# Kernel optimization log

Measured on AMD Instinct MI355X. Metric: run time of the kernel, lower is better.

## Reference

```python
import jax, jax.numpy as jnp
import numpy as np

DIM = 768
HEADS = 12
DH = DIM // HEADS
HIDDEN = 4 * DIM
EPS = 1e-5


def layernorm(x, g, b):
    mu = jnp.mean(x, axis=-1, keepdims=True)
    var = jnp.mean(jnp.square(x - mu), axis=-1, keepdims=True)
    return (x - mu) * jax.lax.rsqrt(var + EPS) * g + b


def setup_inputs() -> dict:
    key = jax.random.key(0)
    ks = jax.random.split(key, 12)
    B, N = 8, 1024
    s_in = 1.0 / np.sqrt(DIM)
    s_hid = 1.0 / np.sqrt(HIDDEN)
    return {
        "x": jax.random.normal(ks[0], (B, N, DIM), jnp.float32),
        "q_extra": jax.random.normal(ks[1], (B, N, DIM), jnp.float32),
        "ln1_g": jnp.ones((DIM,), jnp.float32),
        "ln1_b": jnp.zeros((DIM,), jnp.float32),
        "w_kv": jax.random.normal(ks[2], (DIM, 2 * DIM), jnp.float32) * s_in,
        "w_out": jax.random.normal(ks[3], (DIM, DIM), jnp.float32) * s_in,
        "b_out": jnp.zeros((DIM,), jnp.float32),
        "ln2_g": jnp.ones((DIM,), jnp.float32),
        "ln2_b": jnp.zeros((DIM,), jnp.float32),
        "w1": jax.random.normal(ks[4], (DIM, HIDDEN), jnp.float32) * s_in,
        "b1": jnp.zeros((HIDDEN,), jnp.float32),
        "w2": jax.random.normal(ks[5], (HIDDEN, DIM), jnp.float32) * s_hid,
        "b2": jnp.zeros((DIM,), jnp.float32),
    }


def reference(x, q_extra, ln1_g, ln1_b, w_kv, w_out, b_out, ln2_g, ln2_b, w1, b1, w2, b2):
    B, N, C = x.shape
    scale = DH ** (-0.5)

    # pre-norm cross attention
    xn = layernorm(x, ln1_g, ln1_b)
    kv = (xn @ w_kv).reshape(B, N, 2, HEADS, DH)
    k = kv[:, :, 0]  # [B,N,H,Dh]
    v = kv[:, :, 1]
    q = q_extra.reshape(B, N, HEADS, DH)
    dots = jnp.einsum('bnhd,bmhd->bhnm', q, k) * scale
    attn = jax.nn.softmax(dots, axis=-1)
    out = jnp.einsum('bhnm,bmhd->bnhd', attn, v).reshape(B, N, C)
    out = out @ w_out + b_out

    x = x + out  # residual

    # pre-norm MLP
    h = layernorm(x, ln2_g, ln2_b)
    h = jax.nn.gelu(h @ w1 + b1, approximate=False)
    h = h @ w2 + b2
    return x + h
```

## Files before the change

kernel.cpp:

```cpp
#include <hip/hip_runtime.h>
#include <math.h>

typedef __attribute__((ext_vector_type(8))) short short8;
typedef __attribute__((ext_vector_type(8))) _Float16 half8;
typedef __attribute__((ext_vector_type(2))) __fp16 fp16x2;
typedef __attribute__((ext_vector_type(4))) float float4v;
typedef __attribute__((ext_vector_type(4))) unsigned short ushort4v;

__device__ __forceinline__ unsigned short f2bf(float f) {
  union { unsigned int i; float f; } x; x.f = f;
  unsigned int r = x.i + 0x7fffu + ((x.i >> 16) & 1u);
  return (unsigned short)(r >> 16);
}

__device__ __forceinline__ float gelu_f(float y) {
  const float z = fabsf(y) * 0.70710678118654752f;
  const float t = 1.0f / (1.0f + 0.3275911f * z);
  const float poly = t * (0.254829592f + t * (-0.284496736f +
                     t * (1.421413741f + t * (-1.453152027f + t * 1.061405429f))));
  const float e = exp2f(-z * z * 1.44269504088896f);
  const float erfz = copysignf(1.0f - poly * e, y);
  return 0.5f * y * (1.0f + erfz);
}

__device__ __forceinline__ void ln_row(const float* __restrict__ in,
                                       const float* __restrict__ g,
                                       const float* __restrict__ b,
                                       unsigned short* __restrict__ out,
                                       int row, int lane) {
  const float* xr = in + (size_t)row * 768 + lane * 4;
  const float4 v0 = *(const float4*)(xr);
  const float4 v1 = *(const float4*)(xr + 256);
  const float4 v2 = *(const float4*)(xr + 512);
  float s  = (v0.x + v0.y) + (v0.z + v0.w) + (v1.x + v1.y) + (v1.z + v1.w)
           + (v2.x + v2.y) + (v2.z + v2.w);
  float s2 = v0.x*v0.x + v0.y*v0.y + v0.z*v0.z + v0.w*v0.w
           + v1.x*v1.x + v1.y*v1.y + v1.z*v1.z + v1.w*v1.w
           + v2.x*v2.x + v2.y*v2.y + v2.z*v2.z + v2.w*v2.w;
  for (int off = 32; off > 0; off >>= 1) {
    s  += __shfl_xor(s, off, 64);
    s2 += __shfl_xor(s2, off, 64);
  }
  const float mu = s * (1.0f / 768.0f);
  const float var = s2 * (1.0f / 768.0f) - mu * mu;
  const float rstd = rsqrtf(var + 1e-5f);
  const float* gp = g + lane * 4;
  const float* bp = b + lane * 4;
  unsigned short* orow = out + (size_t)row * 768 + lane * 4;
#pragma unroll
  for (int k = 0; k < 3; ++k) {
    const float4 v = (k == 0) ? v0 : (k == 1) ? v1 : v2;
    const float4 gv = *(const float4*)(gp + k * 256);
    const float4 bv = *(const float4*)(bp + k * 256);
    ushort4v o;
    o.x = f2bf((v.x - mu) * rstd * gv.x + bv.x);
    o.y = f2bf((v.y - mu) * rstd * gv.y + bv.y);
    o.z = f2bf((v.z - mu) * rstd * gv.z + bv.z);
    o.w = f2bf((v.w - mu) * rstd * gv.w + bv.w);
    *(ushort4v*)(orow + k * 256) = o;
  }
}

__global__ void ln_kernel(const float* __restrict__ in, const float* __restrict__ g,
                          const float* __restrict__ b, unsigned short* __restrict__ out) {
  ln_row(in, g, b, out, blockIdx.x * 4 + (threadIdx.x >> 6), threadIdx.x & 63);
}

__device__ __forceinline__ void wtrans_tile(const float* __restrict__ in,
                                            unsigned short* __restrict__ out,
                                            int K, int N, int bx, int by) {
  __shared__ float tile[32][33];
  const int k0 = by * 32, n0 = bx * 32;
  const int tr = threadIdx.x >> 5, tc = threadIdx.x & 31;
#pragma unroll
  for (int i = 0; i < 4; ++i)
    tile[tr + i * 8][tc] = in[(size_t)(k0 + tr + i * 8) * N + n0 + tc];
  __syncthreads();
#pragma unroll
  for (int i = 0; i < 4; ++i)
    out[(size_t)(n0 + tr + i * 8) * K + k0 + tc] = f2bf(tile[tc][tr + i * 8]);
}

__global__ void prep1_kernel(const float* __restrict__ x, const float* __restrict__ g,
                             const float* __restrict__ b, unsigned short* __restrict__ xn,
                             const float* __restrict__ wkv, unsigned short* __restrict__ wkvt,
                             const float* __restrict__ wout, unsigned short* __restrict__ woutt) {
  int id = (int)blockIdx.x;
  if (id < 2048) {
    ln_row(x, g, b, xn, id * 4 + (threadIdx.x >> 6), threadIdx.x & 63);
  } else if (id < 2048 + 1152) {
    id -= 2048;
    wtrans_tile(wkv, wkvt, 768, 1536, id % 48, id / 48);
  } else {
    id -= 2048 + 1152;
    wtrans_tile(wout, woutt, 768, 768, id % 24, id / 24);
  }
}

__global__ void wtrans2_kernel(const float* __restrict__ inA, unsigned short* __restrict__ outA,
                               int KA, int NA, int bxA, int nA,
                               const float* __restrict__ inB, unsigned short* __restrict__ outB,
                               int KB, int NB, int bxB) {
  int id = (int)blockIdx.x;
  if (id < nA) wtrans_tile(inA, outA, KA, NA, id % bxA, id / bxA);
  else { id -= nA; wtrans_tile(inB, outB, KB, NB, id % bxB, id / bxB); }
}

#define SWIZ_BLOCK(GX, TW)                                        \
  const int _id = (int)blockIdx.x;                                \
  const int _gy8 = (int)gridDim.x / (8 * (GX));                   \
  const int _xcd = _id & 7, _jj = _id >> 3;                       \
  const int row0 = (_xcd * _gy8 + _jj / (GX)) * 128;              \
  const int col0 = (_jj % (GX)) * (TW);

#define ASM_FENCE asm volatile("" ::: "memory")

__device__ __forceinline__ void gemm128(
    const unsigned short* __restrict__ A, int lda,
    const unsigned short* __restrict__ Bt, int ldb, int K,
    int row0, int col0,
    unsigned short* As, unsigned short* Bs,
    float4v acc[4][4]) {
  const int t = threadIdx.x, lane = t & 63, wave = t >> 6;
  const int quad = lane >> 4, l16 = lane & 15;
  const int wr = wave >> 1, wc = wave & 1;
  const int srow = lane >> 3;
  const int scol = ((lane & 7) ^ srow) * 8;
#pragma unroll
  for (int mt = 0; mt < 4; ++mt)
#pragma unroll
    for (int nt = 0; nt < 4; ++nt) acc[mt][nt] = (float4v)(0.0f);

  for (int kk = 0; kk < K; kk += 64) {
    __syncthreads();
#pragma unroll
    for (int j = 0; j < 4; ++j) {
      const int chunk = wave * 4 + j;
      const int r = chunk * 8 + srow;
      __builtin_amdgcn_global_load_lds(
          (const __attribute__((address_space(1))) unsigned int*)(A + (size_t)(row0 + r) * lda + kk + scol),
          (__attribute__((address_space(3))) unsigned int*)(As + chunk * 512),
          16, 0, 0);
      __builtin_amdgcn_global_load_lds(
          (const __attribute__((address_space(1))) unsigned int*)(Bt + (size_t)(col0 + r) * ldb + kk + scol),
          (__attribute__((address_space(3))) unsigned int*)(Bs + chunk * 512),
          16, 0, 0);
    }
    __syncthreads();
#pragma unroll
    for (int ks = 0; ks < 2; ++ks) {
      const int gsw = ((ks * 4 + quad) ^ (l16 & 7)) * 8;
      short8 af[4], bfv[4];
#pragma unroll
      for (int i = 0; i < 4; ++i) {
        af[i]  = *(const short8*)(As + (wr * 64 + i * 16 + l16) * 64 + gsw);
        bfv[i] = *(const short8*)(Bs + (wc * 64 + i * 16 + l16) * 64 + gsw);
      }
#pragma unroll
      for (int mt = 0; mt < 4; ++mt)
#pragma unroll
        for (int nt = 0; nt < 4; ++nt)
          acc[mt][nt] = __builtin_amdgcn_mfma_f32_16x16x32_bf16(af[mt], bfv[nt], acc[mt][nt], 0, 0, 0);
    }
  }
}

#define GEMM128_PROLOGUE(GX)                                     \
  __shared__ unsigned short As[128 * 64];                        \
  __shared__ unsigned short Bs[128 * 64];                        \
  float4v acc[4][4];                                             \
  SWIZ_BLOCK(GX, 128)                                            \
  const int t = threadIdx.x, lane = t & 63, wave = t >> 6;       \
  const int quad = lane >> 4, l16 = lane & 15;                   \
  const int wr = wave >> 1, wc = wave & 1; (void)t;

__device__ __forceinline__ void stage12864(
    const unsigned short* __restrict__ A, int lda,
    const unsigned short* __restrict__ Bt, int ldb,
    int row0, int col0, int kk,
    unsigned short* Asb, unsigned short* Bsb,
    int wave, int srow, int scol) {
#pragma unroll
  for (int j = 0; j < 4; ++j) {
    const int chunk = wave * 4 + j;
    const int r = chunk * 8 + srow;
    __builtin_amdgcn_global_load_lds(
        (const __attribute__((address_space(1))) unsigned int*)(A + (size_t)(row0 + r) * lda + kk + scol),
        (__attribute__((address_space(3))) unsigned int*)(Asb + chunk * 512),
        16, 0, 0);
  }
#pragma unroll
  for (int j = 0; j < 2; ++j) {
    const int chunk = wave * 2 + j;
    const int r = chunk * 8 + srow;
    __builtin_amdgcn_global_load_lds(
        (const __attribute__((address_space(1))) unsigned int*)(Bt + (size_t)(col0 + r) * ldb + kk + scol),
        (__attribute__((address_space(3))) unsigned int*)(Bsb + chunk * 512),
        16, 0, 0);
  }
}

__device__ __forceinline__ void mfma_step12864(
    const unsigned short* Ab, const unsigned short* Bb,
    int wave, int quad, int l16, float4v acc[2][4]) {
#pragma unroll
  for (int ks = 0; ks < 2; ++ks) {
    const int gsw = ((ks * 4 + quad) ^ (l16 & 7)) * 8;
    short8 af[2], bfv[4];
#pragma unroll
    for (int i = 0; i < 2; ++i)
      af[i] = *(const short8*)(Ab + (wave * 32 + i * 16 + l16) * 64 + gsw);
#pragma unroll
    for (int i = 0; i < 4; ++i)
      bfv[i] = *(const short8*)(Bb + (i * 16 + l16) * 64 + gsw);
#pragma unroll
    for (int mt = 0; mt < 2; ++mt)
#pragma unroll
      for (int nt = 0; nt < 4; ++nt)
        acc[mt][nt] = __builtin_amdgcn_mfma_f32_16x16x32_bf16(af[mt], bfv[nt], acc[mt][nt], 0, 0, 0);
  }
}

__device__ __forceinline__ void gemm12864(
    const unsigned short* __restrict__ A, int lda,
    const unsigned short* __restrict__ Bt, int ldb, int K,
    int row0, int col0,
    unsigned short* As, unsigned short* Bs,
    float4v acc[2][4]) {
  const int t = threadIdx.x, lane = t & 63, wave = t >> 6;
  const int quad = lane >> 4, l16 = lane & 15;
  const int srow = lane >> 3;
  const int scol = ((lane & 7) ^ srow) * 8;
#pragma unroll
  for (int mt = 0; mt < 2; ++mt)
#pragma unroll
    for (int nt = 0; nt < 4; ++nt) acc[mt][nt] = (float4v)(0.0f);

  stage12864(A, lda, Bt, ldb, row0, col0, 0, As, Bs, wave, srow, scol);
  stage12864(A, lda, Bt, ldb, row0, col0, 64, As + 8192, Bs + 4096, wave, srow, scol);

  for (int kk = 0; kk < K - 128; kk += 128) {
    asm volatile("s_waitcnt vmcnt(6)" ::: "memory");
    __builtin_amdgcn_s_barrier();
    ASM_FENCE;
    mfma_step12864(As, Bs, wave, quad, l16, acc);
    ASM_FENCE;
    __builtin_amdgcn_s_barrier();
    ASM_FENCE;
    stage12864(A, lda, Bt, ldb, row0, col0, kk + 128, As, Bs, wave, srow, scol);

    asm volatile("s_waitcnt vmcnt(6)" ::: "memory");
    __builtin_amdgcn_s_barrier();
    ASM_FENCE;
    mfma_step12864(As + 8192, Bs + 4096, wave, quad, l16, acc);
    ASM_FENCE;
    __builtin_amdgcn_s_barrier();
    ASM_FENCE;
    stage12864(A, lda, Bt, ldb, row0, col0, kk + 192, As + 8192, Bs + 4096, wave, srow, scol);
  }
  asm volatile("s_waitcnt vmcnt(6)" ::: "memory");
  __builtin_amdgcn_s_barrier();
  ASM_FENCE;
  mfma_step12864(As, Bs, wave, quad, l16, acc);
  asm volatile("s_waitcnt vmcnt(0)" ::: "memory");
  __builtin_amdgcn_s_barrier();
  ASM_FENCE;
  mfma_step12864(As + 8192, Bs + 4096, wave, quad, l16, acc);
}

#define GEMM12864_PROLOGUE(GX)                                   \
  __shared__ unsigned short As[2 * 128 * 64];                    \
  __shared__ unsigned short Bs[2 * 64 * 64];                     \
  float4v acc[2][4];                                             \
  SWIZ_BLOCK(GX, 64)                                             \
  const int t = threadIdx.x, lane = t & 63, wave = t >> 6;       \
  const int quad = lane >> 4, l16 = lane & 15; (void)t;

__global__ void gemm_kv_kernel(const unsigned short* __restrict__ xn,
                               const unsigned short* __restrict__ wkvt,
                               _Float16* __restrict__ kbuf,
                               _Float16* __restrict__ vtbuf) {
  GEMM12864_PROLOGUE(24)
  gemm12864(xn, 768, wkvt, 768, 768, row0, col0, As, Bs, acc);
#pragma unroll
  for (int mt = 0; mt < 2; ++mt)
#pragma unroll
    for (int nt = 0; nt < 4; ++nt) {
      const int j = col0 + nt * 16 + l16;
#pragma unroll
      for (int r = 0; r < 4; ++r) {
        const int m = row0 + wave * 32 + mt * 16 + quad * 4 + r;
        const int bb = m >> 10, n = m & 1023;
        const float c = acc[mt][nt][r];
        if (j < 768) {
          const int hh = j >> 6, d = j & 63;
          kbuf[((size_t)(bb * 12 + hh) * 1024 + n) * 64 + d] = (_Float16)c;
        } else {
          const int j2 = j - 768, hh = j2 >> 6, d = j2 & 63;
          vtbuf[((size_t)(bb * 12 + hh) * 64 + d) * 1024 + n] = (_Float16)c;
        }
      }
    }
}

#define AST 72
#define PST 72
__global__ __launch_bounds__(256, 3)
void attn_kernel(const float* __restrict__ q_extra,
                 const _Float16* __restrict__ kbuf,
                 const _Float16* __restrict__ vtbuf,
                 unsigned short* __restrict__ ao) {
  __shared__ _Float16 Ks[64 * AST];
  __shared__ _Float16 Vs[64 * AST];
  __shared__ _Float16 Ps[4][2][16 * PST];
  const int id = (int)blockIdx.x;
  const int pair = id % 96, qb = id / 96;
  const int h = pair >> 3, b = pair & 7;
  const int q0 = qb * 128;
  const int t = threadIdx.x, lane = t & 63, wave = t >> 6;
  const int quad = lane >> 4, l16 = lane & 15;

  const float QS = 0.125f * 1.44269504088896f;
  half8 qf[2][2];
#pragma unroll
  for (int qs = 0; qs < 2; ++qs) {
    const float* qp = q_extra +
        ((size_t)((b * 1024 + q0 + wave * 32 + qs * 16 + l16) * 12 + h)) * 64 + quad * 8;
    float4 a0 = *(const float4*)(qp);
    float4 a1 = *(const float4*)(qp + 4);
    float4 c0 = *(const float4*)(qp + 32);
    float4 c1 = *(const float4*)(qp + 36);
    union { fp16x2 h2[4]; half8 h8; } u0, u1;
    u0.h2[0] = __builtin_amdgcn_cvt_pkrtz(a0.x * QS, a0.y * QS);
    u0.h2[1] = __builtin_amdgcn_cvt_pkrtz(a0.z * QS, a0.w * QS);
    u0.h2[2] = __builtin_amdgcn_cvt_pkrtz(a1.x * QS, a1.y * QS);
    u0.h2[3] = __builtin_amdgcn_cvt_pkrtz(a1.z * QS, a1.w * QS);
    u1.h2[0] = __builtin_amdgcn_cvt_pkrtz(c0.x * QS, c0.y * QS);
    u1.h2[1] = __builtin_amdgcn_cvt_pkrtz(c0.z * QS, c0.w * QS);
    u1.h2[2] = __builtin_amdgcn_cvt_pkrtz(c1.x * QS, c1.y * QS);
    u1.h2[3] = __builtin_amdgcn_cvt_pkrtz(c1.z * QS, c1.w * QS);
    qf[qs][0] = u0.h8; qf[qs][1] = u1.h8;
  }

  const _Float16* kb = kbuf + (size_t)(b * 12 + h) * 65536;
  const _Float16* vb = vtbuf + (size_t)(b * 12 + h) * 65536;
  const int srow = t >> 2, su = (t & 3) * 16;

  half8 kp0 = *(const half8*)(kb + (size_t)srow * 64 + su);
  half8 kp1 = *(const half8*)(kb + (size_t)srow * 64 + su + 8);
  half8 vp0 = *(const half8*)(vb + (size_t)srow * 1024 + su);
  half8 vp1 = *(const half8*)(vb + (size_t)srow * 1024 + su + 8);

  float m_s[2] = {-1e30f, -1e30f}, l_s[2] = {0.0f, 0.0f};
  float4v acc[2][4];
#pragma unroll
  for (int qs = 0; qs < 2; ++qs)
#pragma unroll
    for (int nt = 0; nt < 4; ++nt) acc[qs][nt] = (float4v)(0.0f);

  for (int c = 0; c < 16; ++c) {
    __syncthreads();
    *(half8*)(Ks + srow * AST + su)     = kp0;
    *(half8*)(Ks + srow * AST + su + 8) = kp1;
    *(half8*)(Vs + srow * AST + su)     = vp0;
    *(half8*)(Vs + srow * AST + su + 8) = vp1;
    if (c < 15) {
      const int key1 = (c + 1) * 64;
      kp0 = *(const half8*)(kb + (size_t)(key1 + srow) * 64 + su);
      kp1 = *(const half8*)(kb + (size_t)(key1 + srow) * 64 + su + 8);
      vp0 = *(const half8*)(vb + (size_t)srow * 1024 + key1 + su);
      vp1 = *(const half8*)(vb + (size_t)srow * 1024 + key1 + su + 8);
    }
    __syncthreads();

    float4v s[2][4];
    __builtin_amdgcn_s_setprio(1);
#pragma unroll
    for (int qs = 0; qs < 2; ++qs)
#pragma unroll
      for (int kt = 0; kt < 4; ++kt) {
        const _Float16* kr = Ks + (kt * 16 + l16) * AST;
        half8 kf0 = *(const half8*)(kr + quad * 8);
        half8 kf1 = *(const half8*)(kr + 32 + quad * 8);
        float4v a = (float4v)(0.f);
        a = __builtin_amdgcn_mfma_f32_16x16x32_f16(kf0, qf[qs][0], a, 0, 0, 0);
        a = __builtin_amdgcn_mfma_f32_16x16x32_f16(kf1, qf[qs][1], a, 0, 0, 0);
        s[qs][kt] = a;
      }
    __builtin_amdgcn_s_setprio(0);

#pragma unroll
    for (int qs = 0; qs < 2; ++qs) {
      const float t1 = fmaxf(fmaxf(s[qs][0][0], s[qs][0][1]), s[qs][0][2]);
      const float t2 = fmaxf(fmaxf(s[qs][0][3], s[qs][1][0]), s[qs][1][1]);
      const float t3 = fmaxf(fmaxf(s[qs][1][2], s[qs][1][3]), s[qs][2][0]);
      const float t4 = fmaxf(fmaxf(s[qs][2][1], s[qs][2][2]), s[qs][2][3]);
      const float t5 = fmaxf(fmaxf(s[qs][3][0], s[qs][3][1]), s[qs][3][2]);
      const float mx = fmaxf(fmaxf(fmaxf(t1, t2), t3),
                             fmaxf(fmaxf(t4, t5), s[qs][3][3]));

      if (__any(mx > m_s[qs] + 8.0f)) {
        float gm = fmaxf(mx, __shfl_xor(mx, 16, 64));
        gm = fmaxf(gm, __shfl_xor(gm, 32, 64));
        const float mn = fmaxf(m_s[qs], gm);
        const float alpha = exp2f(m_s[qs] - mn);
        m_s[qs] = mn;
        l_s[qs] *= alpha;
        float ab[4];
#pragma unroll
        for (int r = 0; r < 4; ++r) ab[r] = __shfl(alpha, quad * 4 + r, 64);
#pragma unroll
        for (int nt = 0; nt < 4; ++nt)
#pragma unroll
          for (int r = 0; r < 4; ++r) acc[qs][nt][r] *= ab[r];
      }

      _Float16* pw = Ps[wave][qs];
      float sum = 0.0f;
#pragma unroll
      for (int kt = 0; kt < 4; ++kt) {
        const float p0 = exp2f(s[qs][kt][0] - m_s[qs]);
        const float p1 = exp2f(s[qs][kt][1] - m_s[qs]);
        const float p2 = exp2f(s[qs][kt][2] - m_s[qs]);
        const float p3 = exp2f(s[qs][kt][3] - m_s[qs]);
        sum += (p0 + p1) + (p2 + p3);
        union { fp16x2 h2[2]; uint2 u; } pk;
        pk.h2[0] = __builtin_amdgcn_cvt_pkrtz(p0, p1);
        pk.h2[1] = __builtin_amdgcn_cvt_pkrtz(p2, p3);
        *(uint2*)(pw + l16 * PST + kt * 16 + quad * 4) = pk.u;
      }
      l_s[qs] += sum;
    }

#pragma unroll
    for (int qs = 0; qs < 2; ++qs) {
      _Float16* pw = Ps[wave][qs];
      half8 pf0 = *(const half8*)(pw + l16 * PST + quad * 8);
      half8 pf1 = *(const half8*)(pw + l16 * PST + 32 + quad * 8);
      __builtin_amdgcn_s_setprio(1);
#pragma unroll
      for (int nt = 0; nt < 4; ++nt) {
        const _Float16* vr = Vs + (nt * 16 + l16) * AST;
        half8 vf0 = *(const half8*)(vr + quad * 8);
        half8 vf1 = *(const half8*)(vr + 32 + quad * 8);
        acc[qs][nt] = __builtin_amdgcn_mfma_f32_16x16x32_f16(pf0, vf0, acc[qs][nt], 0, 0, 0);
        acc[qs][nt] = __builtin_amdgcn_mfma_f32_16x16x32_f16(pf1, vf1, acc[qs][nt], 0, 0, 0);
      }
      __builtin_amdgcn_s_setprio(0);
    }
  }

#pragma unroll
  for (int qs = 0; qs < 2; ++qs) {
    l_s[qs] += __shfl_xor(l_s[qs], 16, 64);
    l_s[qs] += __shfl_xor(l_s[qs], 32, 64);
    const float inv = 1.0f / l_s[qs];
    float ib[4];
#pragma unroll
    for (int r = 0; r < 4; ++r) ib[r] = __shfl(inv, quad * 4 + r, 64);
#pragma unroll
    for (int nt = 0; nt < 4; ++nt) {
#pragma unroll
      for (int r = 0; r < 4; ++r) {
        const int m = q0 + wave * 32 + qs * 16 + quad * 4 + r;
        ao[(size_t)(b * 1024 + m) * 768 + h * 64 + nt * 16 + l16] =
            f2bf(acc[qs][nt][r] * ib[r]);
      }
    }
  }
}

__global__ void gemm_outproj_kernel(const unsigned short* __restrict__ ao,
                                    const unsigned short* __restrict__ woutt,
                                    const float* __restrict__ b_out,
                                    const float* __restrict__ x,
                                    float* __restrict__ x2) {
  GEMM12864_PROLOGUE(12)
  gemm12864(ao, 768, woutt, 768, 768, row0, col0, As, Bs, acc);
#pragma unroll
  for (int mt = 0; mt < 2; ++mt)
#pragma unroll
    for (int nt = 0; nt < 4; ++nt) {
      const int j = col0 + nt * 16 + l16;
#pragma unroll
      for (int r = 0; r < 4; ++r) {
        const int m = row0 + wave * 32 + mt * 16 + quad * 4 + r;
        const size_t idx = (size_t)m * 768 + j;
        x2[idx] = acc[mt][nt][r] + b_out[j] + x[idx];
      }
    }
}

__global__ void gemm_mlp1_kernel(const unsigned short* __restrict__ h,
                                 const unsigned short* __restrict__ w1t,
                                 const float* __restrict__ b1,
                                 unsigned short* __restrict__ h1) {
  GEMM128_PROLOGUE(24)
  gemm128(h, 768, w1t, 768, 768, row0, col0, As, Bs, acc);
#pragma unroll
  for (int mt = 0; mt < 4; ++mt)
#pragma unroll
    for (int nt = 0; nt < 4; ++nt) {
      const int j = col0 + wc * 64 + nt * 16 + l16;
#pragma unroll
      for (int r = 0; r < 4; ++r) {
        const int m = row0 + wr * 64 + mt * 16 + quad * 4 + r;
        const float y = acc[mt][nt][r] + b1[j];
        h1[(size_t)m * 3072 + j] = f2bf(gelu_f(y));
      }
    }
}

__global__ void gemm_mlp2_kernel(const unsigned short* __restrict__ h1,
                                 const unsigned short* __restrict__ w2t,
                                 const float* __restrict__ b2,
                                 const float* __restrict__ x2,
                                 float* __restrict__ out) {
  GEMM12864_PROLOGUE(12)
  gemm12864(h1, 3072, w2t, 3072, 3072, row0, col0, As, Bs, acc);
#pragma unroll
  for (int mt = 0; mt < 2; ++mt)
#pragma unroll
    for (int nt = 0; nt < 4; ++nt) {
      const int j = col0 + nt * 16 + l16;
#pragma unroll
      for (int r = 0; r < 4; ++r) {
        const int m = row0 + wave * 32 + mt * 16 + quad * 4 + r;
        const size_t idx = (size_t)m * 768 + j;
        out[idx] = acc[mt][nt][r] + b2[j] + x2[idx];
      }
    }
}

extern "C" void kernel_launch(void* const* d_in, const int* in_sizes, int n_in,
                              void* d_out, int out_size, void* d_ws, size_t ws_size,
                              hipStream_t stream) {
  const float* x       = (const float*)d_in[0];
  const float* q_extra = (const float*)d_in[1];
  const float* ln1_g   = (const float*)d_in[2];
  const float* ln1_b   = (const float*)d_in[3];
  const float* w_kv    = (const float*)d_in[4];
  const float* w_out   = (const float*)d_in[5];
  const float* b_out   = (const float*)d_in[6];
  const float* ln2_g   = (const float*)d_in[7];
  const float* ln2_b   = (const float*)d_in[8];
  const float* w1      = (const float*)d_in[9];
  const float* b1      = (const float*)d_in[10];
  const float* w2      = (const float*)d_in[11];
  const float* b2      = (const float*)d_in[12];
  float* out = (float*)d_out;

  char* ws = (char*)d_ws;
  unsigned short* xn    = (unsigned short*)(ws);
  _Float16*       kbuf  = (_Float16*)(ws + 12582912);
  _Float16*       vtbuf = (_Float16*)(ws + 25165824);
  unsigned short* ao    = (unsigned short*)(ws + 37748736);
  float*          x2    = (float*)(ws + 50331648);
  unsigned short* h1    = (unsigned short*)(ws + 75497472);
  unsigned short* hbuf  = xn;
  unsigned short* wkvt  = ao;
  unsigned short* woutt = h1;
  unsigned short* w1t   = (unsigned short*)kbuf;
  unsigned short* w2t   = (unsigned short*)vtbuf;

  prep1_kernel<<<3776, 256, 0, stream>>>(x, ln1_g, ln1_b, xn,
                                         w_kv, wkvt, w_out, woutt);
  gemm_kv_kernel<<<1536, 256, 0, stream>>>(xn, wkvt, kbuf, vtbuf);
  attn_kernel<<<768, 256, 0, stream>>>(q_extra, kbuf, vtbuf, ao);
  wtrans2_kernel<<<4608, 256, 0, stream>>>(w1, w1t, 768, 3072, 96, 2304,
                                           w2, w2t, 3072, 768, 24);
  gemm_outproj_kernel<<<768, 256, 0, stream>>>(ao, woutt, b_out, x, x2);
  ln_kernel<<<2048, 256, 0, stream>>>(x2, ln2_g, ln2_b, hbuf);
  gemm_mlp1_kernel<<<1536, 256, 0, stream>>>(hbuf, w1t, b1, h1);
  gemm_mlp2_kernel<<<768, 256, 0, stream>>>(h1, w2t, b2, x2, out);
}
```

Before: 363.1 us.

## Split attention block across 8 waves with 16 query rows each

The attention kernel now launches 512 threads per block, and each of the 8 waves handles 16 query rows instead of 4 waves handling 32 rows each. Per-wave registers (accumulators, score tiles, Q fragments) are halved, and each thread loads one K and one V vector per tile instead of two. The aim is more waves in flight per block to hide latency, paid for with more block-wide barriers per unit of work and less K/V fragment reuse per wave.

```diff
diff --git a/kernel.cpp b/kernel.cpp
--- a/kernel.cpp
+++ b/kernel.cpp
@@ -305,14 +305,14 @@
 
 #define AST 72
 #define PST 72
-__global__ __launch_bounds__(256, 3)
+__global__ __launch_bounds__(512, 3)
 void attn_kernel(const float* __restrict__ q_extra,
                  const _Float16* __restrict__ kbuf,
                  const _Float16* __restrict__ vtbuf,
                  unsigned short* __restrict__ ao) {
   __shared__ _Float16 Ks[64 * AST];
   __shared__ _Float16 Vs[64 * AST];
-  __shared__ _Float16 Ps[4][2][16 * PST];
+  __shared__ _Float16 Ps[8][16 * PST];
   const int id = (int)blockIdx.x;
   const int pair = id % 96, qb = id / 96;
   const int h = pair >> 3, b = pair & 7;
@@ -321,11 +321,10 @@
   const int quad = lane >> 4, l16 = lane & 15;
 
   const float QS = 0.125f * 1.44269504088896f;
-  half8 qf[2][2];
-#pragma unroll
-  for (int qs = 0; qs < 2; ++qs) {
+  half8 qf0, qf1;
+  {
     const float* qp = q_extra +
-        ((size_t)((b * 1024 + q0 + wave * 32 + qs * 16 + l16) * 12 + h)) * 64 + quad * 8;
+        ((size_t)((b * 1024 + q0 + wave * 16 + l16) * 12 + h)) * 64 + quad * 8;
     float4 a0 = *(const float4*)(qp);
     float4 a1 = *(const float4*)(qp + 4);
     float4 c0 = *(const float4*)(qp + 32);
@@ -339,133 +338,113 @@
     u1.h2[1] = __builtin_amdgcn_cvt_pkrtz(c0.z * QS, c0.w * QS);
     u1.h2[2] = __builtin_amdgcn_cvt_pkrtz(c1.x * QS, c1.y * QS);
     u1.h2[3] = __builtin_amdgcn_cvt_pkrtz(c1.z * QS, c1.w * QS);
-    qf[qs][0] = u0.h8; qf[qs][1] = u1.h8;
+    qf0 = u0.h8; qf1 = u1.h8;
   }
 
   const _Float16* kb = kbuf + (size_t)(b * 12 + h) * 65536;
   const _Float16* vb = vtbuf + (size_t)(b * 12 + h) * 65536;
-  const int srow = t >> 2, su = (t & 3) * 16;
-
-  half8 kp0 = *(const half8*)(kb + (size_t)srow * 64 + su);
-  half8 kp1 = *(const half8*)(kb + (size_t)srow * 64 + su + 8);
-  half8 vp0 = *(const half8*)(vb + (size_t)srow * 1024 + su);
-  half8 vp1 = *(const half8*)(vb + (size_t)srow * 1024 + su + 8);
-
-  float m_s[2] = {-1e30f, -1e30f}, l_s[2] = {0.0f, 0.0f};
-  float4v acc[2][4];
-#pragma unroll
-  for (int qs = 0; qs < 2; ++qs)
-#pragma unroll
-    for (int nt = 0; nt < 4; ++nt) acc[qs][nt] = (float4v)(0.0f);
+  const int srow = t >> 3, su = (t & 7) * 8;
+
+  half8 kp = *(const half8*)(kb + (size_t)srow * 64 + su);
+  half8 vp = *(const half8*)(vb + (size_t)srow * 1024 + su);
+
+  float m_s = -1e30f, l_s = 0.0f;
+  float4v acc[4];
+#pragma unroll
+  for (int nt = 0; nt < 4; ++nt) acc[nt] = (float4v)(0.0f);
+  _Float16* pw = Ps[wave];
 
   for (int c = 0; c < 16; ++c) {
     __syncthreads();
-    *(half8*)(Ks + srow * AST + su)     = kp0;
-    *(half8*)(Ks + srow * AST + su + 8) = kp1;
-    *(half8*)(Vs + srow * AST + su)     = vp0;
-    *(half8*)(Vs + srow * AST + su + 8) = vp1;
+    *(half8*)(Ks + srow * AST + su) = kp;
+    *(half8*)(Vs + srow * AST + su) = vp;
     if (c < 15) {
       const int key1 = (c + 1) * 64;
-      kp0 = *(const half8*)(kb + (size_t)(key1 + srow) * 64 + su);
-      kp1 = *(const half8*)(kb + (size_t)(key1 + srow) * 64 + su + 8);
-      vp0 = *(const half8*)(vb + (size_t)srow * 1024 + key1 + su);
-      vp1 = *(const half8*)(vb + (size_t)srow * 1024 + key1 + su + 8);
+      kp = *(const half8*)(kb + (size_t)(key1 + srow) * 64 + su);
+      vp = *(const half8*)(vb + (size_t)srow * 1024 + key1 + su);
     }
     __syncthreads();
 
-    float4v s[2][4];
+    float4v s[4];
     __builtin_amdgcn_s_setprio(1);
 #pragma unroll
-    for (int qs = 0; qs < 2; ++qs)
-#pragma unroll
-      for (int kt = 0; kt < 4; ++kt) {
-        const _Float16* kr = Ks + (kt * 16 + l16) * AST;
-        half8 kf0 = *(const half8*)(kr + quad * 8);
-        half8 kf1 = *(const half8*)(kr + 32 + quad * 8);
-        float4v a = (float4v)(0.f);
-        a = __builtin_amdgcn_mfma_f32_16x16x32_f16(kf0, qf[qs][0], a, 0, 0, 0);
-        a = __builtin_amdgcn_mfma_f32_16x16x32_f16(kf1, qf[qs][1], a, 0, 0, 0);
-        s[qs][kt] = a;
-      }
+    for (int kt = 0; kt < 4; ++kt) {
+      const _Float16* kr = Ks + (kt * 16 + l16) * AST;
+      half8 kf0 = *(const half8*)(kr + quad * 8);
+      half8 kf1 = *(const half8*)(kr + 32 + quad * 8);
+      float4v a = (float4v)(0.f);
+      a = __builtin_amdgcn_mfma_f32_16x16x32_f16(kf0, qf0, a, 0, 0, 0);
+      a = __builtin_amdgcn_mfma_f32_16x16x32_f16(kf1, qf1, a, 0, 0, 0);
+      s[kt] = a;
+    }
     __builtin_amdgcn_s_setprio(0);
 
-#pragma unroll
-    for (int qs = 0; qs < 2; ++qs) {
-      const float t1 = fmaxf(fmaxf(s[qs][0][0], s[qs][0][1]), s[qs][0][2]);
-      const float t2 = fmaxf(fmaxf(s[qs][0][3], s[qs][1][0]), s[qs][1][1]);
-      const float t3 = fmaxf(fmaxf(s[qs][1][2], s[qs][1][3]), s[qs][2][0]);
-      const float t4 = fmaxf(fmaxf(s[qs][2][1], s[qs][2][2]), s[qs][2][3]);
-      const float t5 = fmaxf(fmaxf(s[qs][3][0], s[qs][3][1]), s[qs][3][2]);
-      const float mx = fmaxf(fmaxf(fmaxf(t1, t2), t3),
-                             fmaxf(fmaxf(t4, t5), s[qs][3][3]));
-
-      if (__any(mx > m_s[qs] + 8.0f)) {
-        float gm = fmaxf(mx, __shfl_xor(mx, 16, 64));
-        gm = fmaxf(gm, __shfl_xor(gm, 32, 64));
-        const float mn = fmaxf(m_s[qs], gm);
-        const float alpha = exp2f(m_s[qs] - mn);
-        m_s[qs] = mn;
-        l_s[qs] *= alpha;
-        float ab[4];
-#pragma unroll
-        for (int r = 0; r < 4; ++r) ab[r] = __shfl(alpha, quad * 4 + r, 64);
-#pragma unroll
-        for (int nt = 0; nt < 4; ++nt)
-#pragma unroll
-          for (int r = 0; r < 4; ++r) acc[qs][nt][r] *= ab[r];
-      }
-
-      _Float16* pw = Ps[wave][qs];
-      float sum = 0.0f;
-#pragma unroll
-      for (int kt = 0; kt < 4; ++kt) {
-        const float p0 = exp2f(s[qs][kt][0] - m_s[qs]);
-        const float p1 = exp2f(s[qs][kt][1] - m_s[qs]);
-        const float p2 = exp2f(s[qs][kt][2] - m_s[qs]);
-        const float p3 = exp2f(s[qs][kt][3] - m_s[qs]);
-        sum += (p0 + p1) + (p2 + p3);
-        union { fp16x2 h2[2]; uint2 u; } pk;
-        pk.h2[0] = __builtin_amdgcn_cvt_pkrtz(p0, p1);
-        pk.h2[1] = __builtin_amdgcn_cvt_pkrtz(p2, p3);
-        *(uint2*)(pw + l16 * PST + kt * 16 + quad * 4) = pk.u;
-      }
-      l_s[qs] += sum;
-    }
-
-#pragma unroll
-    for (int qs = 0; qs < 2; ++qs) {
-      _Float16* pw = Ps[wave][qs];
-      half8 pf0 = *(const half8*)(pw + l16 * PST + quad * 8);
-      half8 pf1 = *(const half8*)(pw + l16 * PST + 32 + quad * 8);
-      __builtin_amdgcn_s_setprio(1);
-#pragma unroll
-      for (int nt = 0; nt < 4; ++nt) {
-        const _Float16* vr = Vs + (nt * 16 + l16) * AST;
-        half8 vf0 = *(const half8*)(vr + quad * 8);
-        half8 vf1 = *(const half8*)(vr + 32 + quad * 8);
-        acc[qs][nt] = __builtin_amdgcn_mfma_f32_16x16x32_f16(pf0, vf0, acc[qs][nt], 0, 0, 0);
-        acc[qs][nt] = __builtin_amdgcn_mfma_f32_16x16x32_f16(pf1, vf1, acc[qs][nt], 0, 0, 0);
-      }
-      __builtin_amdgcn_s_setprio(0);
-    }
-  }
-
-#pragma unroll
-  for (int qs = 0; qs < 2; ++qs) {
-    l_s[qs] += __shfl_xor(l_s[qs], 16, 64);
-    l_s[qs] += __shfl_xor(l_s[qs], 32, 64);
-    const float inv = 1.0f / l_s[qs];
-    float ib[4];
-#pragma unroll
-    for (int r = 0; r < 4; ++r) ib[r] = __shfl(inv, quad * 4 + r, 64);
+    const float t1 = fmaxf(fmaxf(s[0][0], s[0][1]), s[0][2]);
+    const float t2 = fmaxf(fmaxf(s[0][3], s[1][0]), s[1][1]);
+    const float t3 = fmaxf(fmaxf(s[1][2], s[1][3]), s[2][0]);
+    const float t4 = fmaxf(fmaxf(s[2][1], s[2][2]), s[2][3]);
+    const float t5 = fmaxf(fmaxf(s[3][0], s[3][1]), s[3][2]);
+    const float mx = fmaxf(fmaxf(fmaxf(t1, t2), t3),
+                           fmaxf(fmaxf(t4, t5), s[3][3]));
+
+    if (__any(mx > m_s + 8.0f)) {
+      float gm = fmaxf(mx, __shfl_xor(mx, 16, 64));
+      gm = fmaxf(gm, __shfl_xor(gm, 32, 64));
+      const float mn = fmaxf(m_s, gm);
+      const float alpha = exp2f(m_s - mn);
+      m_s = mn;
+      l_s *= alpha;
+      float ab[4];
+#pragma unroll
+      for (int r = 0; r < 4; ++r) ab[r] = __shfl(alpha, quad * 4 + r, 64);
+#pragma unroll
+      for (int nt = 0; nt < 4; ++nt)
+#pragma unroll
+        for (int r = 0; r < 4; ++r) acc[nt][r] *= ab[r];
+    }
+
+    float sum = 0.0f;
+#pragma unroll
+    for (int kt = 0; kt < 4; ++kt) {
+      const float p0 = exp2f(s[kt][0] - m_s);
+      const float p1 = exp2f(s[kt][1] - m_s);
+      const float p2 = exp2f(s[kt][2] - m_s);
+      const float p3 = exp2f(s[kt][3] - m_s);
+      sum += (p0 + p1) + (p2 + p3);
+      union { fp16x2 h2[2]; uint2 u; } pk;
+      pk.h2[0] = __builtin_amdgcn_cvt_pkrtz(p0, p1);
+      pk.h2[1] = __builtin_amdgcn_cvt_pkrtz(p2, p3);
+      *(uint2*)(pw + l16 * PST + kt * 16 + quad * 4) = pk.u;
+    }
+    l_s += sum;
+
+    half8 pf0 = *(const half8*)(pw + l16 * PST + quad * 8);
+    half8 pf1 = *(const half8*)(pw + l16 * PST + 32 + quad * 8);
+    __builtin_amdgcn_s_setprio(1);
 #pragma unroll
     for (int nt = 0; nt < 4; ++nt) {
-#pragma unroll
-      for (int r = 0; r < 4; ++r) {
-        const int m = q0 + wave * 32 + qs * 16 + quad * 4 + r;
-        ao[(size_t)(b * 1024 + m) * 768 + h * 64 + nt * 16 + l16] =
-            f2bf(acc[qs][nt][r] * ib[r]);
-      }
+      const _Float16* vr = Vs + (nt * 16 + l16) * AST;
+      half8 vf0 = *(const half8*)(vr + quad * 8);
+      half8 vf1 = *(const half8*)(vr + 32 + quad * 8);
+      acc[nt] = __builtin_amdgcn_mfma_f32_16x16x32_f16(pf0, vf0, acc[nt], 0, 0, 0);
+      acc[nt] = __builtin_amdgcn_mfma_f32_16x16x32_f16(pf1, vf1, acc[nt], 0, 0, 0);
+    }
+    __builtin_amdgcn_s_setprio(0);
+  }
+
+  l_s += __shfl_xor(l_s, 16, 64);
+  l_s += __shfl_xor(l_s, 32, 64);
+  const float inv = 1.0f / l_s;
+  float ib[4];
+#pragma unroll
+  for (int r = 0; r < 4; ++r) ib[r] = __shfl(inv, quad * 4 + r, 64);
+#pragma unroll
+  for (int nt = 0; nt < 4; ++nt) {
+#pragma unroll
+    for (int r = 0; r < 4; ++r) {
+      const int m = q0 + wave * 16 + quad * 4 + r;
+      ao[(size_t)(b * 1024 + m) * 768 + h * 64 + nt * 16 + l16] =
+          f2bf(acc[nt][r] * ib[r]);
     }
   }
 }
@@ -566,7 +545,7 @@
   prep1_kernel<<<3776, 256, 0, stream>>>(x, ln1_g, ln1_b, xn,
                                          w_kv, wkvt, w_out, woutt);
   gemm_kv_kernel<<<1536, 256, 0, stream>>>(xn, wkvt, kbuf, vtbuf);
-  attn_kernel<<<768, 256, 0, stream>>>(q_extra, kbuf, vtbuf, ao);
+  attn_kernel<<<768, 512, 0, stream>>>(q_extra, kbuf, vtbuf, ao);
   wtrans2_kernel<<<4608, 256, 0, stream>>>(w1, w1t, 768, 3072, 96, 2304,
                                            w2, w2t, 3072, 768, 24);
   gemm_outproj_kernel<<<768, 256, 0, stream>>>(ao, woutt, b_out, x, x2);
```

New measurement: 347.6 us. -4.3%, faster.
